# Performance work log

Hardware: AMD Instinct MI355X
Metric: run time of the kernel (lower is better)

## Reference

```python
import jax, jax.numpy as jnp
import numpy as np

B, N, H, E, C = 32, 128, 8, 64, 16
D = H * E  # d_model


def auto_head_configs(n_heads, patch_num):
    candidates = set()
    for d in range(1, patch_num + 1):
        for K in (3, 5, 7):
            eff = (K - 1) * d + 1
            if eff <= patch_num and K <= patch_num and (K % 2 == 1):
                candidates.add((K, d, eff))
    gk = patch_num if patch_num % 2 == 1 else patch_num - 1
    gk = max(1, gk)
    candidates.add((gk, 1, gk))
    candidates = sorted(candidates, key=lambda x: (x[2], -x[0], x[1]))
    if not candidates:
        return [(1, 1)] * n_heads
    configs = []
    for h in range(n_heads):
        idx = round(h * (len(candidates) - 1) / max(1, n_heads - 1))
        idx = min(idx, len(candidates) - 1)
        configs.append((candidates[idx][0], candidates[idx][1]))
    return configs


def build_na_mask(n_heads, patch_num):
    mask = np.zeros((n_heads, patch_num, patch_num), dtype=bool)
    for h, (K, d) in enumerate(auto_head_configs(n_heads, patch_num)):
        pos = np.arange(patch_num)[:, None]                      # [N,1]
        ideal = pos + (np.arange(K) - K // 2) * d                # [N,K]
        valid = (ideal >= 0) & (ideal < patch_num)
        rows = np.broadcast_to(pos, ideal.shape)
        mask[h, rows[valid], ideal[valid]] = True
    return mask


def setup_inputs() -> dict:
    key = jax.random.key(0)
    kq, kk, kv, k1, k2 = jax.random.split(key, 5)
    return {
        "queries": jax.random.normal(kq, (B, N, H, E), dtype=jnp.float32),
        "keys": jax.random.normal(kk, (B, C, N, H, E), dtype=jnp.float32),
        "values": jax.random.normal(kv, (B, C, N, H, E), dtype=jnp.float32),
        "w1": jax.random.normal(k1, (D, D // 4), dtype=jnp.float32) * 0.02,
        "b1": jnp.zeros((D // 4,), dtype=jnp.float32),
        "w2": jax.random.normal(k2, (D // 4, 1), dtype=jnp.float32) * 0.02,
        "b2": jnp.zeros((1,), dtype=jnp.float32),
        "na_mask": jnp.asarray(build_na_mask(H, N)),  # [H,N,N] bool
    }


def reference(queries, keys, values, w1, b1, w2, b2, na_mask):
    Bb, Nn, Hh, Ee = queries.shape
    Cc = keys.shape[1]
    scale = Ee ** (-0.5)
    # per-exo-variable gate from mean-pooled values
    v_pool = values.mean(axis=2).reshape(Bb, Cc, Hh * Ee)           # [B,C,D]
    hid = jax.nn.gelu(v_pool @ w1 + b1, approximate=False)
    gate = jax.nn.sigmoid(hid @ w2 + b2)                             # [B,C,1]
    q = queries.transpose(0, 2, 1, 3)                                # [B,H,N,E]
    k_cat = keys.transpose(0, 3, 1, 2, 4).reshape(Bb, Hh, Cc * Nn, Ee)
    v_g = values * gate[:, :, :, None, None]                         # [B,C,N,H,E]
    v_cat = v_g.transpose(0, 3, 1, 2, 4).reshape(Bb, Hh, Cc * Nn, Ee)
    # mask [H,N,N] -> [H,N,C*N] (same neighborhood replicated per exo var)
    tmask = jnp.broadcast_to(na_mask[:, :, None, :], (Hh, Nn, Cc, Nn)).reshape(Hh, Nn, Cc * Nn)
    attn = jnp.einsum('bhne,bhme->bhnm', q, k_cat) * scale
    attn = jnp.where(tmask, attn, -jnp.inf)
    attn = jax.nn.softmax(attn, axis=-1)
    out = jnp.einsum('bhnm,bhme->bhne', attn, v_cat)
    return out.transpose(0, 2, 1, 3)                                 # [B,N,H,E]
```

## Files before the change

kernel.cpp:

```cpp
#include <hip/hip_runtime.h>
#include <hip/hip_bf16.h>
#include <math.h>

#define BB 32
#define NN 128
#define HH 8
#define EE 64
#define CC 16
#define DD 512

#define NEG_BIG (-1.0e30f)

__device__ __forceinline__ float bf2f(unsigned short u) {
    union { unsigned int i; float f; } x; x.i = ((unsigned int)u) << 16; return x.f;
}
__device__ __forceinline__ float bflo(unsigned int u) {
    union { unsigned int i; float f; } x; x.i = u << 16; return x.f;
}
__device__ __forceinline__ float bfhi(unsigned int u) {
    union { unsigned int i; float f; } x; x.i = u & 0xffff0000u; return x.f;
}
__device__ __forceinline__ unsigned short f2bf(float f) {
    union { float f; unsigned int i; } x; x.f = f;
    unsigned int r = x.i + 0x7fffu + ((x.i >> 16) & 1u);
    return (unsigned short)(r >> 16);
}

template <bool F32>
__device__ __forceinline__ float ldx(const void* p, int i) {
    if constexpr (F32) return ((const float*)p)[i];
    else               return bf2f(((const unsigned short*)p)[i]);
}

#define DIL_PACK 0x3F3717250E130501ull

__global__ void detect_dtype(const unsigned short* __restrict__ q, int* __restrict__ flag) {
    const int lane = threadIdx.x;
    int outliers = 0;
    #pragma unroll
    for (int i = 0; i < 16; ++i) {
        unsigned short u = q[(i * 64 + lane) * 2];
        int e = (u >> 7) & 0xFF;
        int sane = (e >= 101 && e <= 140) || ((u & 0x7FFFu) == 0);
        outliers += !sane;
    }
    #pragma unroll
    for (int m = 32; m >= 1; m >>= 1) outliers += __shfl_xor(outliers, m, 64);
    if (lane == 0) *flag = (outliers > 256) ? 1 : 0;
}

template <bool F32>
__device__ __forceinline__ void gate_body(
    const void* __restrict__ values, const void* __restrict__ w1,
    const void* __restrict__ b1, const void* __restrict__ w2,
    const void* __restrict__ b2, float* __restrict__ gate_out,
    float (&vps)[4][DD], float (&vp)[DD], float (&hidp)[4][DD / 4], float (&hid)[DD / 4])
{
    const int bc  = blockIdx.x;
    const int t   = threadIdx.x;
    const int grp = t >> 8;
    const int tt  = t & 255;
    float a0 = 0.f, a1 = 0.f;
    if constexpr (F32) {
        const float2* vb = (const float2*)((const float*)values + (size_t)bc * NN * DD)
                           + (size_t)(grp * 32) * (DD / 2);
        #pragma unroll 8
        for (int n = 0; n < 32; ++n) { float2 u = vb[n * (DD / 2) + tt]; a0 += u.x; a1 += u.y; }
    } else {
        const unsigned int* vb = (const unsigned int*)((const unsigned short*)values + (size_t)bc * NN * DD)
                                 + (size_t)(grp * 32) * (DD / 2);
        #pragma unroll 8
        for (int n = 0; n < 32; ++n) { unsigned int u = vb[n * (DD / 2) + tt]; a0 += bflo(u); a1 += bfhi(u); }
    }
    vps[grp][2 * tt]     = a0;
    vps[grp][2 * tt + 1] = a1;
    __syncthreads();
    if (t < 256) {
        float s0 = vps[0][2 * t]     + vps[1][2 * t]     + vps[2][2 * t]     + vps[3][2 * t];
        float s1 = vps[0][2 * t + 1] + vps[1][2 * t + 1] + vps[2][2 * t + 1] + vps[3][2 * t + 1];
        vp[2 * t]     = s0 * (1.0f / NN);
        vp[2 * t + 1] = s1 * (1.0f / NN);
    }
    __syncthreads();
    if (t < 512) {
        const int o  = t & 127;
        const int ch = t >> 7;
        float a = 0.f;
        #pragma unroll 4
        for (int dd = ch * 128; dd < ch * 128 + 128; ++dd)
            a += vp[dd] * ldx<F32>(w1, dd * (DD / 4) + o);
        hidp[ch][o] = a;
    }
    __syncthreads();
    if (t < 128) {
        float a = ldx<F32>(b1, t) + hidp[0][t] + hidp[1][t] + hidp[2][t] + hidp[3][t];
        hid[t] = 0.5f * a * (1.0f + erff(a * 0.70710678118654752440f));
    }
    __syncthreads();
    if (t < 64) {
        float s = hid[t] * ldx<F32>(w2, t) + hid[t + 64] * ldx<F32>(w2, t + 64);
        #pragma unroll
        for (int m = 32; m >= 1; m >>= 1) s += __shfl_xor(s, m, 64);
        if (t == 0) {
            float z = s + ldx<F32>(b2, 0);
            gate_out[bc] = 1.0f / (1.0f + expf(-z));
        }
    }
}

__global__ __launch_bounds__(1024) void gate_kernel(
    const void* __restrict__ values, const void* __restrict__ w1,
    const void* __restrict__ b1, const void* __restrict__ w2,
    const void* __restrict__ b2, const int* __restrict__ flag,
    float* __restrict__ gate_out)
{
    __shared__ float vps[4][DD];
    __shared__ float vp[DD];
    __shared__ float hidp[4][DD / 4];
    __shared__ float hid[DD / 4];
    if (*flag) gate_body<true >(values, w1, b1, w2, b2, gate_out, vps, vp, hidp, hid);
    else       gate_body<false>(values, w1, b1, w2, b2, gate_out, vps, vp, hidp, hid);
}

template <bool F32, int K>
__device__ __forceinline__ void attn_body(
    const void* __restrict__ qptr, const void* __restrict__ kptr,
    const void* __restrict__ vptr, const float* __restrict__ gate,
    void* __restrict__ optr,
    int b, int h, int n, int dil, int wave, int lane,
    float (&lds_w)[4][CC * 5])
{
    constexpr int nb = CC * K;
    const int g   = lane >> 2;
    const int sub = lane & 3;

    const size_t qoff  = (((size_t)b * NN + n) * HH + h) * EE;
    const size_t kvoff = ((size_t)b * CC * NN) * DD + (size_t)h * EE;

    float qreg[16];
    if constexpr (F32) {
        const float4* qp = (const float4*)((const float*)qptr + qoff + sub * 16);
        #pragma unroll
        for (int i = 0; i < 4; ++i) {
            float4 u = qp[i];
            qreg[4 * i + 0] = u.x * 0.125f; qreg[4 * i + 1] = u.y * 0.125f;
            qreg[4 * i + 2] = u.z * 0.125f; qreg[4 * i + 3] = u.w * 0.125f;
        }
    } else {
        const uint4* qp = (const uint4*)((const unsigned short*)qptr + qoff + sub * 16);
        #pragma unroll
        for (int i = 0; i < 2; ++i) {
            uint4 u = qp[i];
            qreg[8 * i + 0] = bflo(u.x) * 0.125f; qreg[8 * i + 1] = bfhi(u.x) * 0.125f;
            qreg[8 * i + 2] = bflo(u.y) * 0.125f; qreg[8 * i + 3] = bfhi(u.y) * 0.125f;
            qreg[8 * i + 4] = bflo(u.z) * 0.125f; qreg[8 * i + 5] = bfhi(u.z) * 0.125f;
            qreg[8 * i + 6] = bflo(u.w) * 0.125f; qreg[8 * i + 7] = bfhi(u.w) * 0.125f;
        }
    }

    const size_t rowbase = kvoff + (size_t)g * NN * DD + (size_t)sub * 16;
    #pragma unroll
    for (int k = 0; k < K; ++k) {
        int j = n + (k - (K >> 1)) * dil;
        float s = NEG_BIG;
        if (j >= 0 && j < NN) {
            size_t off = rowbase + (size_t)j * DD;
            float a0 = 0.f, a1 = 0.f, a2 = 0.f, a3 = 0.f;
            if constexpr (F32) {
                const float4* kp = (const float4*)((const float*)kptr + off);
                float4 kb[4];
                #pragma unroll
                for (int i = 0; i < 4; ++i) kb[i] = kp[i];
                #pragma unroll
                for (int i = 0; i < 4; ++i) {
                    a0 += qreg[4 * i + 0] * kb[i].x; a1 += qreg[4 * i + 1] * kb[i].y;
                    a2 += qreg[4 * i + 2] * kb[i].z; a3 += qreg[4 * i + 3] * kb[i].w;
                }
            } else {
                const uint4* kp = (const uint4*)((const unsigned short*)kptr + off);
                uint4 kb[2];
                #pragma unroll
                for (int i = 0; i < 2; ++i) kb[i] = kp[i];
                #pragma unroll
                for (int i = 0; i < 2; ++i) {
                    a0 += qreg[8 * i + 0] * bflo(kb[i].x); a1 += qreg[8 * i + 1] * bfhi(kb[i].x);
                    a2 += qreg[8 * i + 2] * bflo(kb[i].y); a3 += qreg[8 * i + 3] * bfhi(kb[i].y);
                    a0 += qreg[8 * i + 4] * bflo(kb[i].z); a1 += qreg[8 * i + 5] * bfhi(kb[i].z);
                    a2 += qreg[8 * i + 6] * bflo(kb[i].w); a3 += qreg[8 * i + 7] * bfhi(kb[i].w);
                }
            }
            s = (a0 + a1) + (a2 + a3);
            s += __shfl_xor(s, 1, 64);
            s += __shfl_xor(s, 2, 64);
        }
        if (sub == 0) lds_w[wave][k * CC + g] = s;
    }
    __syncthreads();

    float s0 = (lane < nb) ? lds_w[wave][lane] : NEG_BIG;
    float s1 = NEG_BIG;
    if constexpr (K == 5) { if (lane < nb - 64) s1 = lds_w[wave][lane + 64]; }
    float m = fmaxf(s0, s1);
    #pragma unroll
    for (int mm = 32; mm >= 1; mm >>= 1) m = fmaxf(m, __shfl_xor(m, mm, 64));
    float e0 = (s0 <= NEG_BIG) ? 0.f : expf(s0 - m);
    float e1 = (s1 <= NEG_BIG) ? 0.f : expf(s1 - m);
    float tsum = e0 + e1;
    #pragma unroll
    for (int mm = 32; mm >= 1; mm >>= 1) tsum += __shfl_xor(tsum, mm, 64);
    float inv = 1.0f / tsum;
    float gv  = gate[b * CC + (lane & 15)];
    lds_w[wave][lane] = e0 * inv * gv;
    if constexpr (K == 5) { if (lane < nb - 64) lds_w[wave][lane + 64] = e1 * inv * gv; }
    __syncthreads();

    float acc = 0.f;
    #pragma unroll
    for (int k = 0; k < K; ++k) {
        int j = n + (k - (K >> 1)) * dil;
        if (j < 0 || j >= NN) continue;
        const float* wrow = lds_w[wave] + k * CC;
        const size_t base = kvoff + (size_t)j * DD + lane;
        float vv[CC];
        if constexpr (F32) {
            const float* vb = (const float*)vptr + base;
            #pragma unroll
            for (int c = 0; c < CC; ++c) vv[c] = vb[(size_t)c * (NN * DD)];
        } else {
            const unsigned short* vb = (const unsigned short*)vptr + base;
            #pragma unroll
            for (int c = 0; c < CC; ++c) vv[c] = bf2f(vb[(size_t)c * (NN * DD)]);
        }
        #pragma unroll
        for (int c = 0; c < CC; ++c) acc += wrow[c] * vv[c];
    }
    if constexpr (F32) ((float*)optr)[qoff + lane] = acc;
    else               ((unsigned short*)optr)[qoff + lane] = f2bf(acc);
}

__global__ __launch_bounds__(256) void attn_kernel(
    const void* __restrict__ qptr, const void* __restrict__ kptr,
    const void* __restrict__ vptr, const float* __restrict__ gate,
    const int* __restrict__ flag, void* __restrict__ optr)
{
    __shared__ float lds_w[4][CC * 5];
    const int tid  = threadIdx.x;
    const int wave = tid >> 6;
    const int lane = tid & 63;

    const int p    = blockIdx.x;
    const int virt = ((p & 7) << 10) | (p >> 3);
    const int gw0  = virt * 4;
    const int n    = (gw0 & (NN - 1)) + wave;
    const int h    = (gw0 >> 7) & (HH - 1);
    const int b    = gw0 >> 10;
    const int dil  = (int)((DIL_PACK >> (h * 8)) & 0xFF);
    const bool k5  = (h & 1) && (h != 7);

    const int f = *flag;
    if (f) {
        if (k5) attn_body<true, 5>(qptr, kptr, vptr, gate, optr, b, h, n, dil, wave, lane, lds_w);
        else    attn_body<true, 3>(qptr, kptr, vptr, gate, optr, b, h, n, dil, wave, lane, lds_w);
    } else {
        if (k5) attn_body<false, 5>(qptr, kptr, vptr, gate, optr, b, h, n, dil, wave, lane, lds_w);
        else    attn_body<false, 3>(qptr, kptr, vptr, gate, optr, b, h, n, dil, wave, lane, lds_w);
    }
}

extern "C" void kernel_launch(void* const* d_in, const int* in_sizes, int n_in,
                              void* d_out, int out_size, void* d_ws, size_t ws_size,
                              hipStream_t stream) {
    const void* queries = d_in[0];
    const void* keys    = d_in[1];
    const void* values  = d_in[2];
    const void* w1      = d_in[3];
    const void* b1      = d_in[4];
    const void* w2      = d_in[5];
    const void* b2      = d_in[6];

    int*   flag    = (int*)d_ws;
    float* gate_ws = (float*)d_ws + 64;

    hipLaunchKernelGGL(detect_dtype, dim3(1), dim3(64), 0, stream,
                       (const unsigned short*)queries, flag);
    hipLaunchKernelGGL(gate_kernel, dim3(BB * CC), dim3(1024), 0, stream,
                       values, w1, b1, w2, b2, flag, gate_ws);
    hipLaunchKernelGGL(attn_kernel, dim3(BB * HH * NN / 4), dim3(256), 0, stream,
                       queries, keys, values, gate_ws, flag, d_out);
}
```

Baseline: 339.0 us.

## Prefetch V rows before softmax, do softmax in registers, drop block barriers

The attention kernel now keeps the per-neighbor scores in registers and runs the softmax with in-wave shuffles, no longer round-tripping them through LDS. The first three neighbors' V rows are loaded before the softmax and the rest right after it, so global-load latency overlaps the softmax math. The two block-wide __syncthreads are replaced by a wave-local LDS wait plus wave barrier. The LDS weight reads are vectorized to float4, and launch bounds now request 4 blocks per CU, which raises register pressure from the prefetched V buffers and risks spills.

After: 339.2 us. About the same (+0.1%).

```diff
diff --git a/kernel.cpp b/kernel.cpp
--- a/kernel.cpp
+++ b/kernel.cpp
@@ -30,6 +30,11 @@
 __device__ __forceinline__ float ldx(const void* p, int i) {
     if constexpr (F32) return ((const float*)p)[i];
     else               return bf2f(((const unsigned short*)p)[i]);
+}
+
+__device__ __forceinline__ void wave_lds_sync() {
+    asm volatile("s_waitcnt lgkmcnt(0)" ::: "memory");
+    __builtin_amdgcn_wave_barrier();
 }
 
 #define DIL_PACK 0x3F3717250E130501ull
@@ -130,12 +135,21 @@
     int b, int h, int n, int dil, int wave, int lane,
     float (&lds_w)[4][CC * 5])
 {
-    constexpr int nb = CC * K;
+    constexpr int PRE = 3;
     const int g   = lane >> 2;
     const int sub = lane & 3;
 
     const size_t qoff  = (((size_t)b * NN + n) * HH + h) * EE;
     const size_t kvoff = ((size_t)b * CC * NN) * DD + (size_t)h * EE;
+
+    int  jj[K];
+    bool va[K];
+    #pragma unroll
+    for (int k = 0; k < K; ++k) {
+        int j = n + (k - (K >> 1)) * dil;
+        va[k] = (j >= 0) && (j < NN);
+        jj[k] = j;
+    }
 
     float qreg[16];
     if constexpr (F32) {
@@ -159,86 +173,129 @@
     }
 
     const size_t rowbase = kvoff + (size_t)g * NN * DD + (size_t)sub * 16;
+    float s[K];
     #pragma unroll
     for (int k = 0; k < K; ++k) {
-        int j = n + (k - (K >> 1)) * dil;
-        float s = NEG_BIG;
-        if (j >= 0 && j < NN) {
-            size_t off = rowbase + (size_t)j * DD;
+        s[k] = NEG_BIG;
+        if (va[k]) {
+            size_t off = rowbase + (size_t)jj[k] * DD;
             float a0 = 0.f, a1 = 0.f, a2 = 0.f, a3 = 0.f;
             if constexpr (F32) {
                 const float4* kp = (const float4*)((const float*)kptr + off);
-                float4 kb[4];
-                #pragma unroll
-                for (int i = 0; i < 4; ++i) kb[i] = kp[i];
                 #pragma unroll
                 for (int i = 0; i < 4; ++i) {
-                    a0 += qreg[4 * i + 0] * kb[i].x; a1 += qreg[4 * i + 1] * kb[i].y;
-                    a2 += qreg[4 * i + 2] * kb[i].z; a3 += qreg[4 * i + 3] * kb[i].w;
+                    float4 kk = kp[i];
+                    a0 += qreg[4 * i + 0] * kk.x; a1 += qreg[4 * i + 1] * kk.y;
+                    a2 += qreg[4 * i + 2] * kk.z; a3 += qreg[4 * i + 3] * kk.w;
                 }
             } else {
                 const uint4* kp = (const uint4*)((const unsigned short*)kptr + off);
-                uint4 kb[2];
-                #pragma unroll
-                for (int i = 0; i < 2; ++i) kb[i] = kp[i];
                 #pragma unroll
                 for (int i = 0; i < 2; ++i) {
-                    a0 += qreg[8 * i + 0] * bflo(kb[i].x); a1 += qreg[8 * i + 1] * bfhi(kb[i].x);
-                    a2 += qreg[8 * i + 2] * bflo(kb[i].y); a3 += qreg[8 * i + 3] * bfhi(kb[i].y);
-                    a0 += qreg[8 * i + 4] * bflo(kb[i].z); a1 += qreg[8 * i + 5] * bfhi(kb[i].z);
-                    a2 += qreg[8 * i + 6] * bflo(kb[i].w); a3 += qreg[8 * i + 7] * bfhi(kb[i].w);
+                    uint4 kk = kp[i];
+                    a0 += qreg[8 * i + 0] * bflo(kk.x); a1 += qreg[8 * i + 1] * bfhi(kk.x);
+                    a2 += qreg[8 * i + 2] * bflo(kk.y); a3 += qreg[8 * i + 3] * bfhi(kk.y);
+                    a0 += qreg[8 * i + 4] * bflo(kk.z); a1 += qreg[8 * i + 5] * bfhi(kk.z);
+                    a2 += qreg[8 * i + 6] * bflo(kk.w); a3 += qreg[8 * i + 7] * bfhi(kk.w);
                 }
             }
-            s = (a0 + a1) + (a2 + a3);
-            s += __shfl_xor(s, 1, 64);
-            s += __shfl_xor(s, 2, 64);
-        }
-        if (sub == 0) lds_w[wave][k * CC + g] = s;
-    }
-    __syncthreads();
-
-    float s0 = (lane < nb) ? lds_w[wave][lane] : NEG_BIG;
-    float s1 = NEG_BIG;
-    if constexpr (K == 5) { if (lane < nb - 64) s1 = lds_w[wave][lane + 64]; }
-    float m = fmaxf(s0, s1);
-    #pragma unroll
-    for (int mm = 32; mm >= 1; mm >>= 1) m = fmaxf(m, __shfl_xor(m, mm, 64));
-    float e0 = (s0 <= NEG_BIG) ? 0.f : expf(s0 - m);
-    float e1 = (s1 <= NEG_BIG) ? 0.f : expf(s1 - m);
-    float tsum = e0 + e1;
-    #pragma unroll
-    for (int mm = 32; mm >= 1; mm >>= 1) tsum += __shfl_xor(tsum, mm, 64);
-    float inv = 1.0f / tsum;
-    float gv  = gate[b * CC + (lane & 15)];
-    lds_w[wave][lane] = e0 * inv * gv;
-    if constexpr (K == 5) { if (lane < nb - 64) lds_w[wave][lane + 64] = e1 * inv * gv; }
-    __syncthreads();
+            float t = (a0 + a1) + (a2 + a3);
+            t += __shfl_xor(t, 1, 64);
+            t += __shfl_xor(t, 2, 64);
+            s[k] = t;
+        }
+    }
+
+    float vv[PRE][CC];
+    #pragma unroll
+    for (int k = 0; k < PRE && k < K; ++k) {
+        if (va[k]) {
+            const size_t base = kvoff + (size_t)jj[k] * DD + lane;
+            if constexpr (F32) {
+                const float* vb = (const float*)vptr + base;
+                #pragma unroll
+                for (int c = 0; c < CC; ++c) vv[k][c] = vb[(size_t)c * (NN * DD)];
+            } else {
+                const unsigned short* vb = (const unsigned short*)vptr + base;
+                #pragma unroll
+                for (int c = 0; c < CC; ++c) vv[k][c] = bf2f(vb[(size_t)c * (NN * DD)]);
+            }
+        }
+    }
+
+    float m = s[0];
+    #pragma unroll
+    for (int k = 1; k < K; ++k) m = fmaxf(m, s[k]);
+    #pragma unroll
+    for (int mm = 4; mm <= 32; mm <<= 1) m = fmaxf(m, __shfl_xor(m, mm, 64));
+    float e[K];
+    float ts = 0.f;
+    #pragma unroll
+    for (int k = 0; k < K; ++k) {
+        if (va[k]) { e[k] = expf(s[k] - m); ts += e[k]; }
+    }
+    #pragma unroll
+    for (int mm = 4; mm <= 32; mm <<= 1) ts += __shfl_xor(ts, mm, 64);
+    float inv = 1.0f / ts;
+    float gv  = gate[b * CC + g];
+    if (sub == 0) {
+        #pragma unroll
+        for (int k = 0; k < K; ++k)
+            if (va[k]) lds_w[wave][k * CC + g] = e[k] * inv * gv;
+    }
+
+    float vl[2][CC];
+    if constexpr (K == 5) {
+        #pragma unroll
+        for (int k = PRE; k < K; ++k) {
+            if (va[k]) {
+                const size_t base = kvoff + (size_t)jj[k] * DD + lane;
+                if constexpr (F32) {
+                    const float* vb = (const float*)vptr + base;
+                    #pragma unroll
+                    for (int c = 0; c < CC; ++c) vl[k - PRE][c] = vb[(size_t)c * (NN * DD)];
+                } else {
+                    const unsigned short* vb = (const unsigned short*)vptr + base;
+                    #pragma unroll
+                    for (int c = 0; c < CC; ++c) vl[k - PRE][c] = bf2f(vb[(size_t)c * (NN * DD)]);
+                }
+            }
+        }
+    }
+
+    wave_lds_sync();
 
     float acc = 0.f;
     #pragma unroll
-    for (int k = 0; k < K; ++k) {
-        int j = n + (k - (K >> 1)) * dil;
-        if (j < 0 || j >= NN) continue;
-        const float* wrow = lds_w[wave] + k * CC;
-        const size_t base = kvoff + (size_t)j * DD + lane;
-        float vv[CC];
-        if constexpr (F32) {
-            const float* vb = (const float*)vptr + base;
-            #pragma unroll
-            for (int c = 0; c < CC; ++c) vv[c] = vb[(size_t)c * (NN * DD)];
-        } else {
-            const unsigned short* vb = (const unsigned short*)vptr + base;
-            #pragma unroll
-            for (int c = 0; c < CC; ++c) vv[c] = bf2f(vb[(size_t)c * (NN * DD)]);
-        }
-        #pragma unroll
-        for (int c = 0; c < CC; ++c) acc += wrow[c] * vv[c];
+    for (int k = 0; k < PRE && k < K; ++k) {
+        if (va[k]) {
+            const float4* w4 = (const float4*)(lds_w[wave] + k * CC);
+            float4 w0 = w4[0], w1 = w4[1], w2 = w4[2], w3 = w4[3];
+            acc += w0.x * vv[k][0]  + w0.y * vv[k][1]  + w0.z * vv[k][2]  + w0.w * vv[k][3];
+            acc += w1.x * vv[k][4]  + w1.y * vv[k][5]  + w1.z * vv[k][6]  + w1.w * vv[k][7];
+            acc += w2.x * vv[k][8]  + w2.y * vv[k][9]  + w2.z * vv[k][10] + w2.w * vv[k][11];
+            acc += w3.x * vv[k][12] + w3.y * vv[k][13] + w3.z * vv[k][14] + w3.w * vv[k][15];
+        }
+    }
+    if constexpr (K == 5) {
+        #pragma unroll
+        for (int k = PRE; k < K; ++k) {
+            if (va[k]) {
+                const float4* w4 = (const float4*)(lds_w[wave] + k * CC);
+                float4 w0 = w4[0], w1 = w4[1], w2 = w4[2], w3 = w4[3];
+                const float* v = vl[k - PRE];
+                acc += w0.x * v[0]  + w0.y * v[1]  + w0.z * v[2]  + w0.w * v[3];
+                acc += w1.x * v[4]  + w1.y * v[5]  + w1.z * v[6]  + w1.w * v[7];
+                acc += w2.x * v[8]  + w2.y * v[9]  + w2.z * v[10] + w2.w * v[11];
+                acc += w3.x * v[12] + w3.y * v[13] + w3.z * v[14] + w3.w * v[15];
+            }
+        }
     }
     if constexpr (F32) ((float*)optr)[qoff + lane] = acc;
     else               ((unsigned short*)optr)[qoff + lane] = f2bf(acc);
 }
 
-__global__ __launch_bounds__(256) void attn_kernel(
+__global__ __launch_bounds__(256, 4) void attn_kernel(
     const void* __restrict__ qptr, const void* __restrict__ kptr,
     const void* __restrict__ vptr, const float* __restrict__ gate,
     const int* __restrict__ flag, void* __restrict__ optr)
```
